# Kernel optimization log

Measured on AMD Instinct MI355X. Metric: run time of the kernel, lower is better.

Reference implementation:

```python
import jax, jax.numpy as jnp
import numpy as np


def setup_inputs() -> dict:
    key = jax.random.key(0)
    B, T, FFT, HOP = 16, 2048, 1024, 256
    n_bins = FFT // 2 + 1  # 513
    stfts = jax.random.normal(key, (B, T, n_bins, 2), dtype=jnp.float32)
    return {"stfts": stfts, "frame_length": FFT, "frame_step": HOP, "fft_length": FFT}


def reference(stfts, frame_length, frame_step, fft_length):
    # --- precomputed constants (built in the layer's build()) ---
    n = jnp.arange(fft_length, dtype=jnp.float32)
    angles = (2.0 * np.pi / fft_length) * (n[:, None] * n[None, :])  # [fft, fft]
    idft_cos = jnp.cos(angles)
    idft_sin = jnp.sin(angles)
    # periodic Hann window
    t = jnp.arange(frame_length, dtype=jnp.float32)
    window = 0.5 - 0.5 * jnp.cos(2.0 * np.pi * t / frame_length)
    hop_ratio = frame_step / frame_length
    normalization = np.sqrt(1.0 / (1.0 - hop_ratio + 1e-8))
    syn_window = window / np.float32(normalization)
    if fft_length > frame_length:
        syn_window = jnp.pad(syn_window, (0, fft_length - frame_length))

    # --- forward ---
    real_part = stfts[..., 0]  # [B, T, n_bins]
    imag_part = stfts[..., 1]
    if fft_length % 2 == 0:
        mirror_real = real_part[:, :, 1:-1]
        mirror_imag = imag_part[:, :, 1:-1]
    else:
        mirror_real = real_part[:, :, 1:]
        mirror_imag = imag_part[:, :, 1:]
    full_real = jnp.concatenate([real_part, mirror_real[:, :, ::-1]], axis=-1)   # [B, T, fft]
    full_imag = jnp.concatenate([imag_part, -mirror_imag[:, :, ::-1]], axis=-1)  # [B, T, fft]

    # explicit IDFT via dense matmul (transpose_b in TF; matrices are symmetric)
    time_real = jnp.einsum('btf,nf->btn', full_real, idft_cos)
    time_real = time_real - jnp.einsum('btf,nf->btn', full_imag, idft_sin)
    time_real = time_real / jnp.float32(fft_length)

    windowed = (time_real * syn_window[None, None, :])[:, :, :frame_length]  # [B, T, frame_length]

    # overlap-and-add
    B, T, L = windowed.shape
    out_len = (T - 1) * frame_step + frame_length
    idx = jnp.arange(T)[:, None] * frame_step + jnp.arange(L)[None, :]  # [T, L]
    out = jnp.zeros((B, out_len), dtype=windowed.dtype).at[:, idx].add(windowed)
    return out
```

## Files before the change

kernel.cpp:

```cpp
#include <hip/hip_runtime.h>
#include <hip/hip_bf16.h>
#include <math.h>


#define BATCH  16
#define TFR    2048
#define NB     513
#define HOP    256
#define OUTLEN 525056
#define RROWS  2051
#define PBR    2054
#define FSTR   1040
#define KTOT   (4 * FSTR)
#define BK     32
#define NKT    (KTOT / BK)
#define KVAL   1026
#define MT     17
#define TOTROW (BATCH * PBR + 128)
#define CHPR   (FSTR / 8)

typedef __attribute__((ext_vector_type(4))) float f32x4;
typedef __attribute__((ext_vector_type(8))) short bf16x8;

__device__ __forceinline__ void load_lds16(const void* g, void* l)
{
    __builtin_amdgcn_global_load_lds((const __attribute__((address_space(1))) void*)g,
                                     (__attribute__((address_space(3))) void*)l,
                                     16, 0, 0);
}

#define STEP 6.13592315e-3f

__global__ __launch_bounds__(256)
void build_B(__hip_bfloat16* __restrict__ Bg)
{
    __shared__ float cosT[1024];
    __shared__ float sinT[1024];
    const int j = blockIdx.x;
    for (int i = threadIdx.x; i < 1024; i += 256) {
        float s, c;
        sincosf((float)i * STEP, &s, &c);
        cosT[i] = c; sinT[i] = s;
    }
    __syncthreads();

    for (int k = threadIdx.x; k < KTOT; k += 256) {
        const int d  = k / FSTR;
        const int kk = k - d * FSTR;
        float val = 0.f;
        if (kk < KVAL) {
            const int   f   = kk >> 1;
            const int   n   = 768 - 256 * d + j;
            const float syn = (0.5f - 0.5f * cosT[n]) * 0.8660254f * (1.0f / 1024.0f);
            const int   idx = (n * f) & 1023;
            if ((kk & 1) == 0) {
                const float wr = (f == 0 || f == 512) ? 1.f : 2.f;
                val = wr * cosT[idx] * syn;
            } else {
                val = -2.f * sinT[idx] * syn;
            }
        }
        Bg[(size_t)j * KTOT + k] = __float2bfloat16(val);
    }
}

__global__ __launch_bounds__(256)
void convert_A(const float* __restrict__ A, __hip_bfloat16* __restrict__ Ab)
{
    const int idx = blockIdx.x * 256 + threadIdx.x;
    if (idx >= TOTROW * CHPR) return;
    const int row = idx / CHPR;
    const int c8  = (idx - row * CHPR) * 8;

    const int b  = row / PBR;
    const int rr = row - b * PBR;
    const bool valid = (b < BATCH) && (rr >= 3) && (rr < 3 + TFR);

    union { bf16x8 v; __hip_bfloat162 h[4]; } u;
    if (valid) {
        const int t = rr - 3;
        const float* src = A + (size_t)(b * TFR + t) * KVAL + c8;
        #pragma unroll
        for (int j = 0; j < 8; j += 2) {
            float2 p = make_float2(0.f, 0.f);
            if (c8 + j < KVAL)
                p = *reinterpret_cast<const float2*>(src + j);
            u.h[j >> 1] = __float22bfloat162_rn(p);
        }
    } else {
        #pragma unroll
        for (int j = 0; j < 4; ++j) u.h[j] = __float22bfloat162_rn(make_float2(0.f, 0.f));
    }
    *reinterpret_cast<bf16x8*>(Ab + (size_t)row * FSTR + c8) = u.v;
}

__global__ __launch_bounds__(256)
void istft_gemm2(const __hip_bfloat16* __restrict__ Ab,
                 const __hip_bfloat16* __restrict__ Bg,
                 float* __restrict__ out)
{
    __shared__ __hip_bfloat16 Asl[128 * BK];
    __shared__ __hip_bfloat16 Bsl[128 * BK];

    const int tid  = threadIdx.x;
    const int bi   = blockIdx.x;
    const int b    = bi / MT;
    const int rt   = (bi - b * MT) * 128;
    const int n0   = blockIdx.y * 128;
    const int lane = tid & 63;
    const int wave = tid >> 6;
    const int wm   = wave >> 1;
    const int wn   = wave & 1;

    f32x4 acc[4][4] = {};

    const int sm = tid >> 2;
    const int sk = (tid & 3) * 8;
    const int fr = lane & 15;
    const int fk = (lane >> 4) * 8;

    const __hip_bfloat16* ga0 = Ab + ((size_t)b * PBR + rt + sm) * FSTR + sk;
    const __hip_bfloat16* ga1 = Ab + ((size_t)b * PBR + rt + 64 + sm) * FSTR + sk;
    const __hip_bfloat16* gb0 = Bg + (size_t)(n0 + sm) * KTOT + sk;
    const __hip_bfloat16* gb1 = Bg + (size_t)(n0 + 64 + sm) * KTOT + sk;

    for (int kt = 0; kt < NKT; ++kt) {
        const int ko = kt * BK;
        load_lds16(ga0 + ko, Asl + tid * 8);
        load_lds16(ga1 + ko, Asl + 2048 + tid * 8);
        load_lds16(gb0 + ko, Bsl + tid * 8);
        load_lds16(gb1 + ko, Bsl + 2048 + tid * 8);
        __syncthreads();

        bf16x8 a[4], bv[4];
        #pragma unroll
        for (int mi = 0; mi < 4; ++mi)
            a[mi] = *reinterpret_cast<const bf16x8*>(&Asl[(wm * 64 + mi * 16 + fr) * BK + fk]);
        #pragma unroll
        for (int ni = 0; ni < 4; ++ni)
            bv[ni] = *reinterpret_cast<const bf16x8*>(&Bsl[(wn * 64 + ni * 16 + fr) * BK + fk]);

        #pragma unroll
        for (int mi = 0; mi < 4; ++mi)
            #pragma unroll
            for (int ni = 0; ni < 4; ++ni)
                acc[mi][ni] = __builtin_amdgcn_mfma_f32_16x16x32_bf16(
                    a[mi], bv[ni], acc[mi][ni], 0, 0, 0);

        __syncthreads();
    }

    const int cr = (lane >> 4) * 4;
    const int cc = lane & 15;
    #pragma unroll
    for (int mi = 0; mi < 4; ++mi) {
        #pragma unroll
        for (int ni = 0; ni < 4; ++ni) {
            const int col = n0 + wn * 64 + ni * 16 + cc;
            #pragma unroll
            for (int j = 0; j < 4; ++j) {
                const int r = rt + wm * 64 + mi * 16 + cr + j;
                if (r < RROWS)
                    out[(size_t)b * OUTLEN + (size_t)r * 256 + col] = acc[mi][ni][j];
            }
        }
    }
}

extern "C" void kernel_launch(void* const* d_in, const int* in_sizes, int n_in,
                              void* d_out, int out_size, void* d_ws, size_t ws_size,
                              hipStream_t stream)
{
    const float* A = reinterpret_cast<const float*>(d_in[0]);
    float* out = reinterpret_cast<float*>(d_out);

    const size_t abBytes = (size_t)TOTROW * FSTR * sizeof(__hip_bfloat16);
    __hip_bfloat16* Ab = reinterpret_cast<__hip_bfloat16*>(d_ws);
    __hip_bfloat16* Bg = reinterpret_cast<__hip_bfloat16*>((char*)d_ws + abBytes);

    build_B<<<dim3(256), dim3(256), 0, stream>>>(Bg);

    const int nChunks = TOTROW * CHPR;
    convert_A<<<dim3((nChunks + 255) / 256), dim3(256), 0, stream>>>(A, Ab);

    istft_gemm2<<<dim3(BATCH * MT, 2), dim3(256), 0, stream>>>(Ab, Bg, out);
}
```

Measured before the change: 235.6 us.

## Use single-wave 64x64 GEMM tiles with double-buffered async LDS loads and XCD-aware mapping

```diff
diff --git a/kernel.cpp b/kernel.cpp
--- a/kernel.cpp
+++ b/kernel.cpp
@@ -15,7 +15,8 @@
 #define BK     32
 #define NKT    (KTOT / BK)
 #define KVAL   1026
-#define MT     17
+#define MTB    33
+#define MTOT   (BATCH * MTB)
 #define TOTROW (BATCH * PBR + 128)
 #define CHPR   (FSTR / 8)
 
@@ -94,51 +95,69 @@
     *reinterpret_cast<bf16x8*>(Ab + (size_t)row * FSTR + c8) = u.v;
 }
 
-__global__ __launch_bounds__(256)
-void istft_gemm2(const __hip_bfloat16* __restrict__ Ab,
+__global__ __launch_bounds__(64)
+void istft_gemm5(const __hip_bfloat16* __restrict__ Ab,
                  const __hip_bfloat16* __restrict__ Bg,
                  float* __restrict__ out)
 {
-    __shared__ __hip_bfloat16 Asl[128 * BK];
-    __shared__ __hip_bfloat16 Bsl[128 * BK];
-
-    const int tid  = threadIdx.x;
-    const int bi   = blockIdx.x;
-    const int b    = bi / MT;
-    const int rt   = (bi - b * MT) * 128;
-    const int n0   = blockIdx.y * 128;
-    const int lane = tid & 63;
-    const int wave = tid >> 6;
-    const int wm   = wave >> 1;
-    const int wn   = wave & 1;
-
-    f32x4 acc[4][4] = {};
-
-    const int sm = tid >> 2;
-    const int sk = (tid & 3) * 8;
+    __shared__ __hip_bfloat16 Asl[2][64 * BK];
+    __shared__ __hip_bfloat16 Bsl[2][64 * BK];
+
+    const int lane = threadIdx.x;
+
+    const int wg   = blockIdx.x;
+    const int xcd  = wg & 7;
+    const int slot = wg >> 3;
+    const int mtg  = xcd * 66 + (slot >> 2);
+    const int nt   = slot & 3;
+
+    const int b  = mtg / MTB;
+    const int rt = (mtg - b * MTB) * 64;
+    const int n0 = nt * 64;
+
+    const int srow = lane >> 2;
+    const int scol = (lane & 3) * 8;
+    const __hip_bfloat16* gA = Ab + ((size_t)b * PBR + rt + srow) * FSTR + scol;
+    const __hip_bfloat16* gB = Bg + (size_t)(n0 + srow) * KTOT + scol;
+
     const int fr = lane & 15;
     const int fk = (lane >> 4) * 8;
 
-    const __hip_bfloat16* ga0 = Ab + ((size_t)b * PBR + rt + sm) * FSTR + sk;
-    const __hip_bfloat16* ga1 = Ab + ((size_t)b * PBR + rt + 64 + sm) * FSTR + sk;
-    const __hip_bfloat16* gb0 = Bg + (size_t)(n0 + sm) * KTOT + sk;
-    const __hip_bfloat16* gb1 = Bg + (size_t)(n0 + 64 + sm) * KTOT + sk;
+    f32x4 acc[4][4] = {};
+
+#define STAGE(buf, kt)                                                          \
+    {                                                                           \
+        const int _ko = (kt) * BK;                                              \
+        _Pragma("unroll")                                                       \
+        for (int _i = 0; _i < 4; ++_i) {                                        \
+            load_lds16(gA + (size_t)_i * 16 * FSTR + _ko,                       \
+                       &Asl[buf][_i * 512 + lane * 8]);                         \
+            load_lds16(gB + (size_t)_i * 16 * KTOT + _ko,                       \
+                       &Bsl[buf][_i * 512 + lane * 8]);                         \
+        }                                                                       \
+    }
+
+    STAGE(0, 0)
+    STAGE(1, 1)
 
     for (int kt = 0; kt < NKT; ++kt) {
-        const int ko = kt * BK;
-        load_lds16(ga0 + ko, Asl + tid * 8);
-        load_lds16(ga1 + ko, Asl + 2048 + tid * 8);
-        load_lds16(gb0 + ko, Bsl + tid * 8);
-        load_lds16(gb1 + ko, Bsl + 2048 + tid * 8);
-        __syncthreads();
-
+        if (kt + 1 < NKT) { asm volatile("s_waitcnt vmcnt(8)" ::: "memory"); }
+        else              { asm volatile("s_waitcnt vmcnt(0)" ::: "memory"); }
+        __builtin_amdgcn_sched_barrier(0);
+
+        const int buf = kt & 1;
         bf16x8 a[4], bv[4];
         #pragma unroll
         for (int mi = 0; mi < 4; ++mi)
-            a[mi] = *reinterpret_cast<const bf16x8*>(&Asl[(wm * 64 + mi * 16 + fr) * BK + fk]);
+            a[mi] = *reinterpret_cast<const bf16x8*>(&Asl[buf][(mi * 16 + fr) * BK + fk]);
         #pragma unroll
         for (int ni = 0; ni < 4; ++ni)
-            bv[ni] = *reinterpret_cast<const bf16x8*>(&Bsl[(wn * 64 + ni * 16 + fr) * BK + fk]);
+            bv[ni] = *reinterpret_cast<const bf16x8*>(&Bsl[buf][(ni * 16 + fr) * BK + fk]);
+
+        asm volatile("s_waitcnt lgkmcnt(0)" ::: "memory");
+        __builtin_amdgcn_sched_barrier(0);
+
+        if (kt + 2 < NKT) STAGE(buf, kt + 2)
 
         #pragma unroll
         for (int mi = 0; mi < 4; ++mi)
@@ -146,9 +165,8 @@
             for (int ni = 0; ni < 4; ++ni)
                 acc[mi][ni] = __builtin_amdgcn_mfma_f32_16x16x32_bf16(
                     a[mi], bv[ni], acc[mi][ni], 0, 0, 0);
-
-        __syncthreads();
-    }
+    }
+#undef STAGE
 
     const int cr = (lane >> 4) * 4;
     const int cc = lane & 15;
@@ -156,10 +174,10 @@
     for (int mi = 0; mi < 4; ++mi) {
         #pragma unroll
         for (int ni = 0; ni < 4; ++ni) {
-            const int col = n0 + wn * 64 + ni * 16 + cc;
+            const int col = n0 + ni * 16 + cc;
             #pragma unroll
             for (int j = 0; j < 4; ++j) {
-                const int r = rt + wm * 64 + mi * 16 + cr + j;
+                const int r = rt + mi * 16 + cr + j;
                 if (r < RROWS)
                     out[(size_t)b * OUTLEN + (size_t)r * 256 + col] = acc[mi][ni][j];
             }
@@ -183,5 +201,5 @@
     const int nChunks = TOTROW * CHPR;
     convert_A<<<dim3((nChunks + 255) / 256), dim3(256), 0, stream>>>(A, Ab);
 
-    istft_gemm2<<<dim3(BATCH * MT, 2), dim3(256), 0, stream>>>(Ab, Bg, out);
-}
+    istft_gemm5<<<dim3(MTOT * 4), dim3(64), 0, stream>>>(Ab, Bg, out);
+}
```

Result: faster. 222.6 us (-5.5%).
